# Kernel tuning notes

Hardware: AMD Instinct MI355X
Metric: run time of the kernel (lower is better)

Reference implementation:

```python
import jax, jax.numpy as jnp
import numpy as np

MEMORY_SIZE = 2000
SHAPE = (512, 8, 8)
D = int(np.prod(SHAPE))  # 32768
LAM = 0.0005  # hard-shrink threshold (1/memory_size convention)
EPS = 1e-12   # F.normalize eps


def _l2_normalize(x, axis):
    # matches F.normalize(p=2): x / max(||x||, eps)
    n = jnp.sqrt(jnp.sum(x * x, axis=axis, keepdims=True))
    return x / jnp.maximum(n, EPS)


def _hard_shrink(x):
    return jnp.where(jnp.abs(x) > LAM, x, jnp.zeros_like(x))


def setup_inputs() -> dict:
    key = jax.random.key(0)
    k1, k2 = jax.random.split(key)
    feature = jax.random.normal(k1, (256, *SHAPE), dtype=jnp.float32)
    memory = jax.random.normal(k2, (MEMORY_SIZE, D), dtype=jnp.float32)
    return {"feature": feature, "memory": memory}


def reference(feature, memory):
    B = feature.shape[0]
    flat = feature.reshape(B, -1)                     # [B, D]
    fn = _l2_normalize(flat, axis=1)                  # [B, D]
    mn = _l2_normalize(memory, axis=1)                # [M, D]
    w = jnp.einsum('bd,md->bm', fn, mn)               # cosine similarity [B, M]
    w = jax.nn.softmax(w, axis=1)
    w = _hard_shrink(w)
    w = jax.nn.softmax(w, axis=1)
    mem_feat = jnp.einsum('bm,md->bd', w, memory)     # [B, D]
    mem_feat = mem_feat.reshape(B, *SHAPE)
    return (mem_feat, w)
```

## Files before the change

kernel.cpp:

```cpp
#include <hip/hip_runtime.h>
#include <math.h>


#define D_DIM 32768
#define B_DIM 256
#define M_DIM 2000
#define M_PAD 2048
#define NSPLIT 16
#define LAM 0.0005f
#define LDA 72

typedef __attribute__((ext_vector_type(8))) short bf16x8;
typedef __attribute__((ext_vector_type(4))) float f32x4;

__device__ __forceinline__ unsigned short f2bf(float f) {
  union { float f; unsigned u; } v; v.f = f;
  unsigned r = v.u + 0x7FFFu + ((v.u >> 16) & 1u);
  return (unsigned short)(r >> 16);
}

__global__ __launch_bounds__(256) void prep_kernel(const float* __restrict__ src,
                                                   unsigned short* __restrict__ dst,
                                                   float* __restrict__ rn_inv) {
  const size_t row = blockIdx.x;
  const int t = threadIdx.x;
  const float4* p = (const float4*)(src + row * (size_t)D_DIM);
  ushort4* q = (ushort4*)(dst + row * (size_t)D_DIM);
  float s = 0.f;
  for (int i = t; i < D_DIM / 4; i += 256) {
    float4 v = p[i];
    s = fmaf(v.x, v.x, s); s = fmaf(v.y, v.y, s);
    s = fmaf(v.z, v.z, s); s = fmaf(v.w, v.w, s);
    ushort4 b; b.x = f2bf(v.x); b.y = f2bf(v.y); b.z = f2bf(v.z); b.w = f2bf(v.w);
    q[i] = b;
  }
  #pragma unroll
  for (int off = 32; off > 0; off >>= 1) s += __shfl_down(s, off, 64);
  __shared__ float partial[4];
  if ((t & 63) == 0) partial[t >> 6] = s;
  __syncthreads();
  if (t == 0) {
    float tt = partial[0] + partial[1] + partial[2] + partial[3];
    rn_inv[row] = 1.0f / fmaxf(sqrtf(tt), 1e-12f);
  }
}

__global__ __launch_bounds__(256) void gemm1_kernel(const unsigned short* __restrict__ A,
                                                    const unsigned short* __restrict__ Bm,
                                                    float* __restrict__ Spart) {
  __shared__ __align__(16) unsigned short Asm[256 * LDA];
  __shared__ __align__(16) unsigned short Bsm[64 * LDA];
  const int t = threadIdx.x;
  const int n0 = blockIdx.x * 64;
  const int kbase = blockIdx.y * (D_DIM / NSPLIT);
  const int wid = t >> 6, lane = t & 63;
  const int lr = lane & 15, kq = lane >> 4;
  const int sr = t >> 3;
  const int sc = (t & 7) * 8;

  f32x4 acc[4][4] = {};

  for (int kk = 0; kk < D_DIM / NSPLIT; kk += 64) {
    const size_t kg = (size_t)(kbase + kk + sc);
    __syncthreads();
    #pragma unroll
    for (int i = 0; i < 8; i++) {
      const int r = sr + 32 * i;
      const bf16x8 v = *(const bf16x8*)(A + (size_t)r * D_DIM + kg);
      *(bf16x8*)&Asm[r * LDA + sc] = v;
    }
    #pragma unroll
    for (int i = 0; i < 2; i++) {
      const int r = sr + 32 * i;
      const bf16x8 v = *(const bf16x8*)(Bm + (size_t)(n0 + r) * D_DIM + kg);
      *(bf16x8*)&Bsm[r * LDA + sc] = v;
    }
    __syncthreads();
    bf16x8 bfr[4][2];
    #pragma unroll
    for (int ni = 0; ni < 4; ni++)
      #pragma unroll
      for (int h = 0; h < 2; h++)
        bfr[ni][h] = *(const bf16x8*)&Bsm[(ni * 16 + lr) * LDA + h * 32 + kq * 8];
    #pragma unroll
    for (int mi = 0; mi < 4; mi++) {
      #pragma unroll
      for (int h = 0; h < 2; h++) {
        const bf16x8 af = *(const bf16x8*)&Asm[(wid * 64 + mi * 16 + lr) * LDA + h * 32 + kq * 8];
        #pragma unroll
        for (int ni = 0; ni < 4; ni++)
          acc[mi][ni] = __builtin_amdgcn_mfma_f32_16x16x32_bf16(af, bfr[ni][h], acc[mi][ni], 0, 0, 0);
      }
    }
  }
  float* Sp = Spart + (size_t)blockIdx.y * (B_DIM * M_PAD);
  #pragma unroll
  for (int mi = 0; mi < 4; mi++) {
    const int row0 = wid * 64 + mi * 16 + kq * 4;
    #pragma unroll
    for (int ni = 0; ni < 4; ni++) {
      const int col = n0 + ni * 16 + lr;
      #pragma unroll
      for (int j = 0; j < 4; j++)
        Sp[(size_t)(row0 + j) * M_PAD + col] = acc[mi][ni][j];
    }
  }
}

__device__ __forceinline__ float block_reduce(float x, bool is_max, float* red,
                                              int wid, int lane) {
  #pragma unroll
  for (int off = 32; off > 0; off >>= 1) {
    float o = __shfl_down(x, off, 64);
    x = is_max ? fmaxf(x, o) : (x + o);
  }
  __syncthreads();
  if (lane == 0) red[wid] = x;
  __syncthreads();
  return is_max ? fmaxf(fmaxf(red[0], red[1]), fmaxf(red[2], red[3]))
                : (red[0] + red[1] + red[2] + red[3]);
}

__global__ __launch_bounds__(256) void softmax_kernel(const float* __restrict__ Spart,
                                                      const float* __restrict__ rnf,
                                                      const float* __restrict__ rnm,
                                                      float* __restrict__ wout,
                                                      unsigned short* __restrict__ wbf) {
  const int b = blockIdx.x;
  const int t = threadIdx.x;
  const int wid = t >> 6, lane = t & 63;
  const float sf = rnf[b];
  __shared__ float red[4];

  float v[8];
  #pragma unroll
  for (int i = 0; i < 8; i++) {
    const int m = t + 256 * i;
    float a = 0.f;
    #pragma unroll
    for (int s = 0; s < NSPLIT; s++)
      a += Spart[(size_t)s * (B_DIM * M_PAD) + (size_t)b * M_PAD + m];
    v[i] = (m < M_DIM) ? a * (sf * rnm[m]) : -INFINITY;
  }
  float mx = v[0];
  #pragma unroll
  for (int i = 1; i < 8; i++) mx = fmaxf(mx, v[i]);
  mx = block_reduce(mx, true, red, wid, lane);

  float e[8]; float sum = 0.f;
  #pragma unroll
  for (int i = 0; i < 8; i++) { e[i] = expf(v[i] - mx); sum += e[i]; }
  sum = block_reduce(sum, false, red, wid, lane);
  const float inv = 1.f / sum;

  float s2[8];
  #pragma unroll
  for (int i = 0; i < 8; i++) {
    float w1 = e[i] * inv;
    s2[i] = (w1 > LAM) ? w1 : 0.f;
  }
  float mx2 = 0.f;
  #pragma unroll
  for (int i = 0; i < 8; i++) mx2 = fmaxf(mx2, s2[i]);
  mx2 = block_reduce(mx2, true, red, wid, lane);

  float e2[8]; float sum2 = 0.f;
  #pragma unroll
  for (int i = 0; i < 8; i++) {
    const int m = t + 256 * i;
    e2[i] = (m < M_DIM) ? expf(s2[i] - mx2) : 0.f;
    sum2 += e2[i];
  }
  sum2 = block_reduce(sum2, false, red, wid, lane);
  const float inv2 = 1.f / sum2;

  #pragma unroll
  for (int i = 0; i < 8; i++) {
    const int m = t + 256 * i;
    const float w2 = e2[i] * inv2;
    if (m < M_DIM) wout[(size_t)b * M_DIM + m] = w2;
    wbf[(size_t)b * M_PAD + m] = f2bf(w2);
  }
}

__global__ __launch_bounds__(256) void gemm2_kernel(const unsigned short* __restrict__ W,
                                                    const unsigned short* __restrict__ Bm,
                                                    float* __restrict__ C) {
  __shared__ __align__(16) unsigned short Wsm[256 * LDA];
  __shared__ __align__(16) unsigned short Bt[64 * LDA];
  const int t = threadIdx.x;
  const int n0 = blockIdx.x * 64;
  const int wid = t >> 6, lane = t & 63;
  const int lr = lane & 15, kq = lane >> 4;
  const int sr = t >> 3, sc = (t & 7) * 8;
  const int bk = t >> 4;
  const int bnc = (t & 15) * 4;

  f32x4 acc[4][4] = {};

  for (int k0 = 0; k0 < M_PAD; k0 += 64) {
    __syncthreads();
    #pragma unroll
    for (int i = 0; i < 8; i++) {
      const int r = sr + 32 * i;
      const bf16x8 v = *(const bf16x8*)(W + (size_t)r * M_PAD + k0 + sc);
      *(bf16x8*)&Wsm[r * LDA + sc] = v;
    }
    #pragma unroll
    for (int i = 0; i < 4; i++) {
      const int kl = bk + 16 * i;
      const ushort4 v = *(const ushort4*)(Bm + (size_t)(k0 + kl) * D_DIM + n0 + bnc);
      Bt[(bnc + 0) * LDA + kl] = v.x;
      Bt[(bnc + 1) * LDA + kl] = v.y;
      Bt[(bnc + 2) * LDA + kl] = v.z;
      Bt[(bnc + 3) * LDA + kl] = v.w;
    }
    __syncthreads();
    bf16x8 bfr[4][2];
    #pragma unroll
    for (int ni = 0; ni < 4; ni++)
      #pragma unroll
      for (int h = 0; h < 2; h++)
        bfr[ni][h] = *(const bf16x8*)&Bt[(ni * 16 + lr) * LDA + h * 32 + kq * 8];
    #pragma unroll
    for (int mi = 0; mi < 4; mi++) {
      #pragma unroll
      for (int h = 0; h < 2; h++) {
        const bf16x8 af = *(const bf16x8*)&Wsm[(wid * 64 + mi * 16 + lr) * LDA + h * 32 + kq * 8];
        #pragma unroll
        for (int ni = 0; ni < 4; ni++)
          acc[mi][ni] = __builtin_amdgcn_mfma_f32_16x16x32_bf16(af, bfr[ni][h], acc[mi][ni], 0, 0, 0);
      }
    }
  }
  #pragma unroll
  for (int mi = 0; mi < 4; mi++) {
    const int row0 = wid * 64 + mi * 16 + kq * 4;
    #pragma unroll
    for (int ni = 0; ni < 4; ni++) {
      const int col = n0 + ni * 16 + lr;
      #pragma unroll
      for (int j = 0; j < 4; j++)
        C[(size_t)(row0 + j) * D_DIM + col] = acc[mi][ni][j];
    }
  }
}

extern "C" void kernel_launch(void* const* d_in, const int* in_sizes, int n_in,
                              void* d_out, int out_size, void* d_ws, size_t ws_size,
                              hipStream_t stream) {
  const float* feature = (const float*)d_in[0];
  const float* memory  = (const float*)d_in[1];
  float* out_feat = (float*)d_out;
  float* out_w = out_feat + (size_t)B_DIM * D_DIM;

  char* ws = (char*)d_ws;
  unsigned short* Mem16 = (unsigned short*)ws;
  unsigned short* F16   = (unsigned short*)(ws + 134217728);
  float* Spart          = (float*)(ws + 150994944);
  unsigned short* Wbf   = (unsigned short*)(ws + 184549376);
  float* rnm            = (float*)(ws + 185597952);
  float* rnf            = (float*)(ws + 185606144);

  prep_kernel<<<M_DIM, 256, 0, stream>>>(memory, Mem16, rnm);
  prep_kernel<<<B_DIM, 256, 0, stream>>>(feature, F16, rnf);
  gemm1_kernel<<<dim3(32, NSPLIT), 256, 0, stream>>>(F16, Mem16, Spart);
  softmax_kernel<<<B_DIM, 256, 0, stream>>>(Spart, rnf, rnm, out_w, Wbf);
  gemm2_kernel<<<D_DIM / 64, 256, 0, stream>>>(Wbf, Mem16, out_feat);
}
```

Before: 563.0 us.

## Pre-transpose memory for GEMM2 and use swizzled async global-to-LDS loads

Memory preprocessing is now a tiled kernel that writes both the row-major bf16 copy and a transposed (D x M_PAD) bf16 copy. Row norms are accumulated with atomics into a squared-norm buffer that a new zero kernel clears first. Both GEMMs share a core that loads tiles with global_load_lds 16-byte async copies into XOR-swizzled unpadded LDS. This removes GEMM2's scalar LDS transpose, and the split-K count for GEMM1 is doubled. The trade-off is an extra 128MB transposed write in prep, a larger partial-sum buffer for softmax to reduce, and the reliance on the gfx950 LDS-load intrinsic.

```diff
diff --git a/kernel.cpp b/kernel.cpp
--- a/kernel.cpp
+++ b/kernel.cpp
@@ -6,12 +6,19 @@
 #define B_DIM 256
 #define M_DIM 2000
 #define M_PAD 2048
-#define NSPLIT 16
+#define NSPLIT 32
 #define LAM 0.0005f
-#define LDA 72
 
 typedef __attribute__((ext_vector_type(8))) short bf16x8;
 typedef __attribute__((ext_vector_type(4))) float f32x4;
+
+#define GLOBAL_AS __attribute__((address_space(1)))
+#define LDS_AS __attribute__((address_space(3)))
+
+__device__ __forceinline__ void cp_async16(const void* g, void* l) {
+  __builtin_amdgcn_global_load_lds((const GLOBAL_AS unsigned int*)g,
+                                   (LDS_AS unsigned int*)l, 16, 0, 0);
+}
 
 __device__ __forceinline__ unsigned short f2bf(float f) {
   union { float f; unsigned u; } v; v.f = f;
@@ -19,9 +26,14 @@
   return (unsigned short)(r >> 16);
 }
 
-__global__ __launch_bounds__(256) void prep_kernel(const float* __restrict__ src,
-                                                   unsigned short* __restrict__ dst,
-                                                   float* __restrict__ rn_inv) {
+__global__ __launch_bounds__(256) void zero_kernel(float* __restrict__ p, int n) {
+  int i = blockIdx.x * 256 + threadIdx.x;
+  if (i < n) p[i] = 0.f;
+}
+
+__global__ __launch_bounds__(256) void prep_feat_kernel(const float* __restrict__ src,
+                                                        unsigned short* __restrict__ dst,
+                                                        float* __restrict__ rn_inv) {
   const size_t row = blockIdx.x;
   const int t = threadIdx.x;
   const float4* p = (const float4*)(src + row * (size_t)D_DIM);
@@ -45,54 +57,120 @@
   }
 }
 
+#define LT_S 70
+__global__ __launch_bounds__(256) void prep_mem_kernel(const float* __restrict__ src,
+                                                       unsigned short* __restrict__ Mem16,
+                                                       unsigned short* __restrict__ MemT,
+                                                       float* __restrict__ rnm_sq) {
+  __shared__ __align__(16) unsigned short LT[64 * LT_S];
+  const int t = threadIdx.x;
+  const int m0 = blockIdx.y * 64;
+  const int d0 = blockIdx.x * 256;
+  const int rrow = t >> 4;
+  const int c4 = (t & 15) * 4;
+  float nacc[4] = {0.f, 0.f, 0.f, 0.f};
+
+  for (int sub = 0; sub < 4; sub++) {
+    const int d = d0 + sub * 64;
+    __syncthreads();
+    #pragma unroll
+    for (int p = 0; p < 4; p++) {
+      const int mr = rrow + 16 * p;
+      const int m = m0 + mr;
+      float4 v = make_float4(0.f, 0.f, 0.f, 0.f);
+      if (m < M_DIM) v = *(const float4*)(src + (size_t)m * D_DIM + d + c4);
+      nacc[p] = fmaf(v.x, v.x, fmaf(v.y, v.y, fmaf(v.z, v.z, fmaf(v.w, v.w, nacc[p]))));
+      ushort4 b; b.x = f2bf(v.x); b.y = f2bf(v.y); b.z = f2bf(v.z); b.w = f2bf(v.w);
+      *(ushort4*)&Mem16[(size_t)m * D_DIM + d + c4] = b;
+      *(ushort4*)&LT[mr * LT_S + c4] = b;
+    }
+    __syncthreads();
+    #pragma unroll
+    for (int p = 0; p < 4; p++) {
+      const int dl = rrow + 16 * p;
+      ushort4 o;
+      o.x = LT[(c4 + 0) * LT_S + dl];
+      o.y = LT[(c4 + 1) * LT_S + dl];
+      o.z = LT[(c4 + 2) * LT_S + dl];
+      o.w = LT[(c4 + 3) * LT_S + dl];
+      *(ushort4*)&MemT[(size_t)(d + dl) * M_PAD + m0 + c4] = o;
+    }
+  }
+  #pragma unroll
+  for (int p = 0; p < 4; p++) {
+    float s = nacc[p];
+    #pragma unroll
+    for (int off = 8; off > 0; off >>= 1) s += __shfl_down(s, off, 16);
+    if ((t & 15) == 0) {
+      const int m = m0 + rrow + 16 * p;
+      if (m < M_DIM) atomicAdd(&rnm_sq[m], s);
+    }
+  }
+}
+
+template <int KTILES>
+__device__ __forceinline__ void gemm_core(const unsigned short* __restrict__ A,
+                                          const unsigned short* __restrict__ B,
+                                          size_t lda, size_t ldb,
+                                          unsigned short* Asm, unsigned short* Bsm,
+                                          f32x4 acc[4][4]) {
+  const int t = threadIdx.x;
+  const int wid = t >> 6, lane = t & 63;
+  const int lr = lane & 15, kq = lane >> 4;
+  const int l8 = lane & 7, lrow = lane >> 3;
+  const int sw_stage = (l8 ^ lrow) * 8;
+
+  const unsigned short* Ab = A + (size_t)(64 * wid + lrow) * lda + sw_stage;
+  const unsigned short* Bb = B + (size_t)(16 * wid + lrow) * ldb + sw_stage;
+
+  for (int kt = 0; kt < KTILES; kt++) {
+    const int kk = kt * 64;
+    __syncthreads();
+    #pragma unroll
+    for (int i = 0; i < 8; i++)
+      cp_async16(Ab + kk + (size_t)(8 * i) * lda, &Asm[(64 * wid + 8 * i) * 64]);
+    #pragma unroll
+    for (int i = 0; i < 2; i++)
+      cp_async16(Bb + kk + (size_t)(8 * i) * ldb, &Bsm[(16 * wid + 8 * i) * 64]);
+    __syncthreads();
+
+    bf16x8 bfr[2][4];
+    #pragma unroll
+    for (int h = 0; h < 2; h++) {
+      const int sw = ((h * 4 + kq) ^ (lr & 7)) * 8;
+      #pragma unroll
+      for (int ni = 0; ni < 4; ni++)
+        bfr[h][ni] = *(const bf16x8*)&Bsm[(ni * 16 + lr) * 64 + sw];
+    }
+    #pragma unroll
+    for (int mi = 0; mi < 4; mi++) {
+      #pragma unroll
+      for (int h = 0; h < 2; h++) {
+        const int sw = ((h * 4 + kq) ^ (lr & 7)) * 8;
+        const bf16x8 af = *(const bf16x8*)&Asm[(wid * 64 + mi * 16 + lr) * 64 + sw];
+        #pragma unroll
+        for (int ni = 0; ni < 4; ni++)
+          acc[mi][ni] = __builtin_amdgcn_mfma_f32_16x16x32_bf16(af, bfr[h][ni], acc[mi][ni], 0, 0, 0);
+      }
+    }
+  }
+}
+
 __global__ __launch_bounds__(256) void gemm1_kernel(const unsigned short* __restrict__ A,
                                                     const unsigned short* __restrict__ Bm,
                                                     float* __restrict__ Spart) {
-  __shared__ __align__(16) unsigned short Asm[256 * LDA];
-  __shared__ __align__(16) unsigned short Bsm[64 * LDA];
+  __shared__ __align__(16) unsigned short Asm[256 * 64];
+  __shared__ __align__(16) unsigned short Bsm[64 * 64];
   const int t = threadIdx.x;
   const int n0 = blockIdx.x * 64;
   const int kbase = blockIdx.y * (D_DIM / NSPLIT);
   const int wid = t >> 6, lane = t & 63;
   const int lr = lane & 15, kq = lane >> 4;
-  const int sr = t >> 3;
-  const int sc = (t & 7) * 8;
 
   f32x4 acc[4][4] = {};
-
-  for (int kk = 0; kk < D_DIM / NSPLIT; kk += 64) {
-    const size_t kg = (size_t)(kbase + kk + sc);
-    __syncthreads();
-    #pragma unroll
-    for (int i = 0; i < 8; i++) {
-      const int r = sr + 32 * i;
-      const bf16x8 v = *(const bf16x8*)(A + (size_t)r * D_DIM + kg);
-      *(bf16x8*)&Asm[r * LDA + sc] = v;
-    }
-    #pragma unroll
-    for (int i = 0; i < 2; i++) {
-      const int r = sr + 32 * i;
-      const bf16x8 v = *(const bf16x8*)(Bm + (size_t)(n0 + r) * D_DIM + kg);
-      *(bf16x8*)&Bsm[r * LDA + sc] = v;
-    }
-    __syncthreads();
-    bf16x8 bfr[4][2];
-    #pragma unroll
-    for (int ni = 0; ni < 4; ni++)
-      #pragma unroll
-      for (int h = 0; h < 2; h++)
-        bfr[ni][h] = *(const bf16x8*)&Bsm[(ni * 16 + lr) * LDA + h * 32 + kq * 8];
-    #pragma unroll
-    for (int mi = 0; mi < 4; mi++) {
-      #pragma unroll
-      for (int h = 0; h < 2; h++) {
-        const bf16x8 af = *(const bf16x8*)&Asm[(wid * 64 + mi * 16 + lr) * LDA + h * 32 + kq * 8];
-        #pragma unroll
-        for (int ni = 0; ni < 4; ni++)
-          acc[mi][ni] = __builtin_amdgcn_mfma_f32_16x16x32_bf16(af, bfr[ni][h], acc[mi][ni], 0, 0, 0);
-      }
-    }
-  }
+  gemm_core<(D_DIM / NSPLIT) / 64>(A + kbase, Bm + (size_t)n0 * D_DIM + kbase,
+                                   D_DIM, D_DIM, Asm, Bsm, acc);
+
   float* Sp = Spart + (size_t)blockIdx.y * (B_DIM * M_PAD);
   #pragma unroll
   for (int mi = 0; mi < 4; mi++) {
@@ -107,6 +185,32 @@
   }
 }
 
+__global__ __launch_bounds__(256) void gemm2_kernel(const unsigned short* __restrict__ W,
+                                                    const unsigned short* __restrict__ Bt,
+                                                    float* __restrict__ C) {
+  __shared__ __align__(16) unsigned short Asm[256 * 64];
+  __shared__ __align__(16) unsigned short Bsm[64 * 64];
+  const int t = threadIdx.x;
+  const int n0 = blockIdx.x * 64;
+  const int wid = t >> 6, lane = t & 63;
+  const int lr = lane & 15, kq = lane >> 4;
+
+  f32x4 acc[4][4] = {};
+  gemm_core<M_PAD / 64>(W, Bt + (size_t)n0 * M_PAD, M_PAD, M_PAD, Asm, Bsm, acc);
+
+  #pragma unroll
+  for (int mi = 0; mi < 4; mi++) {
+    const int row0 = wid * 64 + mi * 16 + kq * 4;
+    #pragma unroll
+    for (int ni = 0; ni < 4; ni++) {
+      const int col = n0 + ni * 16 + lr;
+      #pragma unroll
+      for (int j = 0; j < 4; j++)
+        C[(size_t)(row0 + j) * D_DIM + col] = acc[mi][ni][j];
+    }
+  }
+}
+
 __device__ __forceinline__ float block_reduce(float x, bool is_max, float* red,
                                               int wid, int lane) {
   #pragma unroll
@@ -123,7 +227,7 @@
 
 __global__ __launch_bounds__(256) void softmax_kernel(const float* __restrict__ Spart,
                                                       const float* __restrict__ rnf,
-                                                      const float* __restrict__ rnm,
+                                                      const float* __restrict__ rnm_sq,
                                                       float* __restrict__ wout,
                                                       unsigned short* __restrict__ wbf) {
   const int b = blockIdx.x;
@@ -140,7 +244,8 @@
     #pragma unroll
     for (int s = 0; s < NSPLIT; s++)
       a += Spart[(size_t)s * (B_DIM * M_PAD) + (size_t)b * M_PAD + m];
-    v[i] = (m < M_DIM) ? a * (sf * rnm[m]) : -INFINITY;
+    const float mscale = 1.0f / fmaxf(sqrtf(rnm_sq[m]), 1e-12f);
+    v[i] = (m < M_DIM) ? a * (sf * mscale) : -INFINITY;
   }
   float mx = v[0];
   #pragma unroll
@@ -180,69 +285,6 @@
     const float w2 = e2[i] * inv2;
     if (m < M_DIM) wout[(size_t)b * M_DIM + m] = w2;
     wbf[(size_t)b * M_PAD + m] = f2bf(w2);
-  }
-}
-
-__global__ __launch_bounds__(256) void gemm2_kernel(const unsigned short* __restrict__ W,
-                                                    const unsigned short* __restrict__ Bm,
-                                                    float* __restrict__ C) {
-  __shared__ __align__(16) unsigned short Wsm[256 * LDA];
-  __shared__ __align__(16) unsigned short Bt[64 * LDA];
-  const int t = threadIdx.x;
-  const int n0 = blockIdx.x * 64;
-  const int wid = t >> 6, lane = t & 63;
-  const int lr = lane & 15, kq = lane >> 4;
-  const int sr = t >> 3, sc = (t & 7) * 8;
-  const int bk = t >> 4;
-  const int bnc = (t & 15) * 4;
-
-  f32x4 acc[4][4] = {};
-
-  for (int k0 = 0; k0 < M_PAD; k0 += 64) {
-    __syncthreads();
-    #pragma unroll
-    for (int i = 0; i < 8; i++) {
-      const int r = sr + 32 * i;
-      const bf16x8 v = *(const bf16x8*)(W + (size_t)r * M_PAD + k0 + sc);
-      *(bf16x8*)&Wsm[r * LDA + sc] = v;
-    }
-    #pragma unroll
-    for (int i = 0; i < 4; i++) {
-      const int kl = bk + 16 * i;
-      const ushort4 v = *(const ushort4*)(Bm + (size_t)(k0 + kl) * D_DIM + n0 + bnc);
-      Bt[(bnc + 0) * LDA + kl] = v.x;
-      Bt[(bnc + 1) * LDA + kl] = v.y;
-      Bt[(bnc + 2) * LDA + kl] = v.z;
-      Bt[(bnc + 3) * LDA + kl] = v.w;
-    }
-    __syncthreads();
-    bf16x8 bfr[4][2];
-    #pragma unroll
-    for (int ni = 0; ni < 4; ni++)
-      #pragma unroll
-      for (int h = 0; h < 2; h++)
-        bfr[ni][h] = *(const bf16x8*)&Bt[(ni * 16 + lr) * LDA + h * 32 + kq * 8];
-    #pragma unroll
-    for (int mi = 0; mi < 4; mi++) {
-      #pragma unroll
-      for (int h = 0; h < 2; h++) {
-        const bf16x8 af = *(const bf16x8*)&Wsm[(wid * 64 + mi * 16 + lr) * LDA + h * 32 + kq * 8];
-        #pragma unroll
-        for (int ni = 0; ni < 4; ni++)
-          acc[mi][ni] = __builtin_amdgcn_mfma_f32_16x16x32_bf16(af, bfr[ni][h], acc[mi][ni], 0, 0, 0);
-      }
-    }
-  }
-  #pragma unroll
-  for (int mi = 0; mi < 4; mi++) {
-    const int row0 = wid * 64 + mi * 16 + kq * 4;
-    #pragma unroll
-    for (int ni = 0; ni < 4; ni++) {
-      const int col = n0 + ni * 16 + lr;
-      #pragma unroll
-      for (int j = 0; j < 4; j++)
-        C[(size_t)(row0 + j) * D_DIM + col] = acc[mi][ni][j];
-    }
   }
 }
 
@@ -256,15 +298,17 @@
 
   char* ws = (char*)d_ws;
   unsigned short* Mem16 = (unsigned short*)ws;
-  unsigned short* F16   = (unsigned short*)(ws + 134217728);
-  float* Spart          = (float*)(ws + 150994944);
-  unsigned short* Wbf   = (unsigned short*)(ws + 184549376);
-  float* rnm            = (float*)(ws + 185597952);
-  float* rnf            = (float*)(ws + 185606144);
-
-  prep_kernel<<<M_DIM, 256, 0, stream>>>(memory, Mem16, rnm);
-  prep_kernel<<<B_DIM, 256, 0, stream>>>(feature, F16, rnf);
-  gemm1_kernel<<<dim3(32, NSPLIT), 256, 0, stream>>>(F16, Mem16, Spart);
-  softmax_kernel<<<B_DIM, 256, 0, stream>>>(Spart, rnf, rnm, out_w, Wbf);
-  gemm2_kernel<<<D_DIM / 64, 256, 0, stream>>>(Wbf, Mem16, out_feat);
-}
+  unsigned short* MemT  = (unsigned short*)(ws + 134217728ull);
+  unsigned short* F16   = (unsigned short*)(ws + 268435456ull);
+  unsigned short* Wbf   = (unsigned short*)(ws + 285212672ull);
+  float* Spart          = (float*)(ws + 286261248ull);
+  float* rnm_sq         = (float*)(ws + 353370112ull);
+  float* rnf            = (float*)(ws + 353378304ull);
+
+  zero_kernel<<<(M_PAD + 255) / 256, 256, 0, stream>>>(rnm_sq, M_PAD);
+  prep_feat_kernel<<<B_DIM, 256, 0, stream>>>(feature, F16, rnf);
+  prep_mem_kernel<<<dim3(D_DIM / 256, 32), 256, 0, stream>>>(memory, Mem16, MemT, rnm_sq);
+  gemm1_kernel<<<dim3(M_PAD / 64, NSPLIT), 256, 0, stream>>>(F16, Mem16, Spart);
+  softmax_kernel<<<B_DIM, 256, 0, stream>>>(Spart, rnf, rnm_sq, out_w, Wbf);
+  gemm2_kernel<<<D_DIM / 64, 256, 0, stream>>>(Wbf, MemT, out_feat);
+}
```

New measurement: 613.1 us. 1.09x slower.

## Fuse memory bf16 conversion and norm into GEMM1, add async LDS loads

Applied to the files above, without the earlier changes.

The separate prep pass over the fp32 memory matrix is removed. GEMM1 now reads fp32 memory directly, converts it to bf16 in registers, writes the bf16 copy for GEMM2, and accumulates squared row norms with atomics that the softmax kernel turns into inverse norms. The activation and weight tiles in both GEMMs are loaded with global_load_lds into an XOR-swizzled unpadded LDS layout. GEMM2's transpose stores now pack pairs of k values into 32-bit LDS writes. The aim is to avoid re-reading the bf16 memory copy and to cut load-instruction and LDS-store overhead, at the cost of heavier fp32 traffic inside GEMM1, atomic norm accumulation, and an extra zeroing launch.

```diff
diff --git a/kernel.cpp b/kernel.cpp
--- a/kernel.cpp
+++ b/kernel.cpp
@@ -6,12 +6,21 @@
 #define B_DIM 256
 #define M_DIM 2000
 #define M_PAD 2048
-#define NSPLIT 16
+#define NS1 16
+#define KSLAB (D_DIM / NS1)
 #define LAM 0.0005f
-#define LDA 72
+#define LDB 72
 
 typedef __attribute__((ext_vector_type(8))) short bf16x8;
 typedef __attribute__((ext_vector_type(4))) float f32x4;
+
+#define GLOBAL_AS __attribute__((address_space(1)))
+#define LDS_AS __attribute__((address_space(3)))
+
+__device__ __forceinline__ void cp_async16(const void* g, void* l) {
+  __builtin_amdgcn_global_load_lds((const GLOBAL_AS unsigned int*)g,
+                                   (LDS_AS unsigned int*)l, 16, 0, 0);
+}
 
 __device__ __forceinline__ unsigned short f2bf(float f) {
   union { float f; unsigned u; } v; v.f = f;
@@ -19,9 +28,14 @@
   return (unsigned short)(r >> 16);
 }
 
-__global__ __launch_bounds__(256) void prep_kernel(const float* __restrict__ src,
-                                                   unsigned short* __restrict__ dst,
-                                                   float* __restrict__ rn_inv) {
+__global__ __launch_bounds__(256) void zero_kernel(float* __restrict__ p, int n) {
+  int i = blockIdx.x * 256 + threadIdx.x;
+  if (i < n) p[i] = 0.f;
+}
+
+__global__ __launch_bounds__(256) void prep_feat_kernel(const float* __restrict__ src,
+                                                        unsigned short* __restrict__ dst,
+                                                        float* __restrict__ rn_inv) {
   const size_t row = blockIdx.x;
   const int t = threadIdx.x;
   const float4* p = (const float4*)(src + row * (size_t)D_DIM);
@@ -45,64 +59,94 @@
   }
 }
 
-__global__ __launch_bounds__(256) void gemm1_kernel(const unsigned short* __restrict__ A,
-                                                    const unsigned short* __restrict__ Bm,
-                                                    float* __restrict__ Spart) {
-  __shared__ __align__(16) unsigned short Asm[256 * LDA];
-  __shared__ __align__(16) unsigned short Bsm[64 * LDA];
+__global__ __launch_bounds__(256) void gemm1_fused(const unsigned short* __restrict__ F16,
+                                                   const float* __restrict__ mem,
+                                                   unsigned short* __restrict__ Mem16,
+                                                   float* __restrict__ Spart,
+                                                   float* __restrict__ rnm_sq) {
+  __shared__ __align__(16) unsigned short Asm[256 * 64];
+  __shared__ __align__(16) unsigned short Bsm[64 * LDB];
   const int t = threadIdx.x;
-  const int n0 = blockIdx.x * 64;
-  const int kbase = blockIdx.y * (D_DIM / NSPLIT);
+  const int m0 = blockIdx.x * 64;
+  const int kbase = blockIdx.y * KSLAB;
   const int wid = t >> 6, lane = t & 63;
   const int lr = lane & 15, kq = lane >> 4;
-  const int sr = t >> 3;
-  const int sc = (t & 7) * 8;
+  const int l8 = lane & 7, lrow = lane >> 3;
+
+  const int brow = t >> 2;
+  const int bcol = (t & 3) * 16;
+  const int gm = m0 + brow;
+  const bool bvalid = gm < M_DIM;
+  const float* Bg = mem + (size_t)gm * D_DIM + kbase + bcol;
+  unsigned short* M16g = Mem16 + (size_t)gm * D_DIM + kbase + bcol;
+
+  const unsigned short* Ab = F16 + (size_t)(64 * wid + lrow) * D_DIM + kbase + (l8 ^ lrow) * 8;
 
   f32x4 acc[4][4] = {};
-
-  for (int kk = 0; kk < D_DIM / NSPLIT; kk += 64) {
-    const size_t kg = (size_t)(kbase + kk + sc);
+  float ss = 0.f;
+
+  for (int kt = 0; kt < KSLAB / 64; kt++) {
+    const int kk = kt * 64;
     __syncthreads();
     #pragma unroll
-    for (int i = 0; i < 8; i++) {
-      const int r = sr + 32 * i;
-      const bf16x8 v = *(const bf16x8*)(A + (size_t)r * D_DIM + kg);
-      *(bf16x8*)&Asm[r * LDA + sc] = v;
-    }
-    #pragma unroll
-    for (int i = 0; i < 2; i++) {
-      const int r = sr + 32 * i;
-      const bf16x8 v = *(const bf16x8*)(Bm + (size_t)(n0 + r) * D_DIM + kg);
-      *(bf16x8*)&Bsm[r * LDA + sc] = v;
-    }
+    for (int i = 0; i < 8; i++)
+      cp_async16(Ab + kk + (size_t)(8 * i) * D_DIM, &Asm[(64 * wid + 8 * i) * 64]);
+
+    float4 v[4];
+    #pragma unroll
+    for (int j = 0; j < 4; j++)
+      v[j] = bvalid ? *(const float4*)(Bg + kk + 4 * j) : make_float4(0.f, 0.f, 0.f, 0.f);
+    ushort4 c[4];
+    #pragma unroll
+    for (int j = 0; j < 4; j++) {
+      ss = fmaf(v[j].x, v[j].x, ss); ss = fmaf(v[j].y, v[j].y, ss);
+      ss = fmaf(v[j].z, v[j].z, ss); ss = fmaf(v[j].w, v[j].w, ss);
+      c[j].x = f2bf(v[j].x); c[j].y = f2bf(v[j].y);
+      c[j].z = f2bf(v[j].z); c[j].w = f2bf(v[j].w);
+    }
+    *(ushort4*)&Bsm[brow * LDB + bcol + 0]  = c[0];
+    *(ushort4*)&Bsm[brow * LDB + bcol + 4]  = c[1];
+    *(ushort4*)&Bsm[brow * LDB + bcol + 8]  = c[2];
+    *(ushort4*)&Bsm[brow * LDB + bcol + 12] = c[3];
+    *(ushort4*)(M16g + kk + 0)  = c[0];
+    *(ushort4*)(M16g + kk + 4)  = c[1];
+    *(ushort4*)(M16g + kk + 8)  = c[2];
+    *(ushort4*)(M16g + kk + 12) = c[3];
     __syncthreads();
-    bf16x8 bfr[4][2];
-    #pragma unroll
-    for (int ni = 0; ni < 4; ni++)
-      #pragma unroll
-      for (int h = 0; h < 2; h++)
-        bfr[ni][h] = *(const bf16x8*)&Bsm[(ni * 16 + lr) * LDA + h * 32 + kq * 8];
+
+    bf16x8 bfr[2][4];
+    #pragma unroll
+    for (int h = 0; h < 2; h++)
+      #pragma unroll
+      for (int ni = 0; ni < 4; ni++)
+        bfr[h][ni] = *(const bf16x8*)&Bsm[(ni * 16 + lr) * LDB + h * 32 + kq * 8];
     #pragma unroll
     for (int mi = 0; mi < 4; mi++) {
       #pragma unroll
       for (int h = 0; h < 2; h++) {
-        const bf16x8 af = *(const bf16x8*)&Asm[(wid * 64 + mi * 16 + lr) * LDA + h * 32 + kq * 8];
+        const int sw = ((h * 4 + kq) ^ (lr & 7)) * 8;
+        const bf16x8 af = *(const bf16x8*)&Asm[(wid * 64 + mi * 16 + lr) * 64 + sw];
         #pragma unroll
         for (int ni = 0; ni < 4; ni++)
-          acc[mi][ni] = __builtin_amdgcn_mfma_f32_16x16x32_bf16(af, bfr[ni][h], acc[mi][ni], 0, 0, 0);
+          acc[mi][ni] = __builtin_amdgcn_mfma_f32_16x16x32_bf16(af, bfr[h][ni], acc[mi][ni], 0, 0, 0);
       }
     }
   }
+
+  ss += __shfl_down(ss, 2, 4);
+  ss += __shfl_down(ss, 1, 4);
+  if ((t & 3) == 0 && bvalid) atomicAdd(&rnm_sq[gm], ss);
+
   float* Sp = Spart + (size_t)blockIdx.y * (B_DIM * M_PAD);
   #pragma unroll
   for (int mi = 0; mi < 4; mi++) {
-    const int row0 = wid * 64 + mi * 16 + kq * 4;
+    const int b0 = wid * 64 + mi * 16 + kq * 4;
     #pragma unroll
     for (int ni = 0; ni < 4; ni++) {
-      const int col = n0 + ni * 16 + lr;
+      const int col = m0 + ni * 16 + lr;
       #pragma unroll
       for (int j = 0; j < 4; j++)
-        Sp[(size_t)(row0 + j) * M_PAD + col] = acc[mi][ni][j];
+        Sp[(size_t)(b0 + j) * M_PAD + col] = acc[mi][ni][j];
     }
   }
 }
@@ -123,7 +167,7 @@
 
 __global__ __launch_bounds__(256) void softmax_kernel(const float* __restrict__ Spart,
                                                       const float* __restrict__ rnf,
-                                                      const float* __restrict__ rnm,
+                                                      const float* __restrict__ rnm_sq,
                                                       float* __restrict__ wout,
                                                       unsigned short* __restrict__ wbf) {
   const int b = blockIdx.x;
@@ -138,9 +182,10 @@
     const int m = t + 256 * i;
     float a = 0.f;
     #pragma unroll
-    for (int s = 0; s < NSPLIT; s++)
+    for (int s = 0; s < NS1; s++)
       a += Spart[(size_t)s * (B_DIM * M_PAD) + (size_t)b * M_PAD + m];
-    v[i] = (m < M_DIM) ? a * (sf * rnm[m]) : -INFINITY;
+    const float mscale = 1.0f / fmaxf(sqrtf(rnm_sq[m]), 1e-12f);
+    v[i] = (m < M_DIM) ? a * (sf * mscale) : -INFINITY;
   }
   float mx = v[0];
   #pragma unroll
@@ -186,62 +231,69 @@
 __global__ __launch_bounds__(256) void gemm2_kernel(const unsigned short* __restrict__ W,
                                                     const unsigned short* __restrict__ Bm,
                                                     float* __restrict__ C) {
-  __shared__ __align__(16) unsigned short Wsm[256 * LDA];
-  __shared__ __align__(16) unsigned short Bt[64 * LDA];
+  __shared__ __align__(16) unsigned short Wsm[256 * 64];
+  __shared__ __align__(16) unsigned short Bt[64 * LDB];
   const int t = threadIdx.x;
   const int n0 = blockIdx.x * 64;
   const int wid = t >> 6, lane = t & 63;
   const int lr = lane & 15, kq = lane >> 4;
-  const int sr = t >> 3, sc = (t & 7) * 8;
-  const int bk = t >> 4;
-  const int bnc = (t & 15) * 4;
+  const int l8 = lane & 7, lrow = lane >> 3;
+
+  const unsigned short* Wb = W + (size_t)(64 * wid + lrow) * M_PAD + (l8 ^ lrow) * 8;
+
+  const int kl2 = 2 * (t >> 4);
+  const int d4 = (t & 15) * 4;
 
   f32x4 acc[4][4] = {};
 
   for (int k0 = 0; k0 < M_PAD; k0 += 64) {
     __syncthreads();
     #pragma unroll
-    for (int i = 0; i < 8; i++) {
-      const int r = sr + 32 * i;
-      const bf16x8 v = *(const bf16x8*)(W + (size_t)r * M_PAD + k0 + sc);
-      *(bf16x8*)&Wsm[r * LDA + sc] = v;
-    }
-    #pragma unroll
-    for (int i = 0; i < 4; i++) {
-      const int kl = bk + 16 * i;
-      const ushort4 v = *(const ushort4*)(Bm + (size_t)(k0 + kl) * D_DIM + n0 + bnc);
-      Bt[(bnc + 0) * LDA + kl] = v.x;
-      Bt[(bnc + 1) * LDA + kl] = v.y;
-      Bt[(bnc + 2) * LDA + kl] = v.z;
-      Bt[(bnc + 3) * LDA + kl] = v.w;
+    for (int i = 0; i < 8; i++)
+      cp_async16(Wb + k0 + (size_t)(8 * i) * M_PAD, &Wsm[(64 * wid + 8 * i) * 64]);
+    #pragma unroll
+    for (int it = 0; it < 2; it++) {
+      const int kl = kl2 + 32 * it;
+      const ushort4 va = *(const ushort4*)(Bm + (size_t)(k0 + kl) * D_DIM + n0 + d4);
+      const ushort4 vb = *(const ushort4*)(Bm + (size_t)(k0 + kl + 1) * D_DIM + n0 + d4);
+      const unsigned p0 = (unsigned)va.x | ((unsigned)vb.x << 16);
+      const unsigned p1 = (unsigned)va.y | ((unsigned)vb.y << 16);
+      const unsigned p2 = (unsigned)va.z | ((unsigned)vb.z << 16);
+      const unsigned p3 = (unsigned)va.w | ((unsigned)vb.w << 16);
+      *(unsigned*)&Bt[(d4 + 0) * LDB + kl] = p0;
+      *(unsigned*)&Bt[(d4 + 1) * LDB + kl] = p1;
+      *(unsigned*)&Bt[(d4 + 2) * LDB + kl] = p2;
+      *(unsigned*)&Bt[(d4 + 3) * LDB + kl] = p3;
     }
     __syncthreads();
-    bf16x8 bfr[4][2];
-    #pragma unroll
-    for (int ni = 0; ni < 4; ni++)
-      #pragma unroll
-      for (int h = 0; h < 2; h++)
-        bfr[ni][h] = *(const bf16x8*)&Bt[(ni * 16 + lr) * LDA + h * 32 + kq * 8];
+
+    bf16x8 bfr[2][4];
+    #pragma unroll
+    for (int h = 0; h < 2; h++)
+      #pragma unroll
+      for (int ni = 0; ni < 4; ni++)
+        bfr[h][ni] = *(const bf16x8*)&Bt[(ni * 16 + lr) * LDB + h * 32 + kq * 8];
     #pragma unroll
     for (int mi = 0; mi < 4; mi++) {
       #pragma unroll
       for (int h = 0; h < 2; h++) {
-        const bf16x8 af = *(const bf16x8*)&Wsm[(wid * 64 + mi * 16 + lr) * LDA + h * 32 + kq * 8];
+        const int sw = ((h * 4 + kq) ^ (lr & 7)) * 8;
+        const bf16x8 af = *(const bf16x8*)&Wsm[(wid * 64 + mi * 16 + lr) * 64 + sw];
         #pragma unroll
         for (int ni = 0; ni < 4; ni++)
-          acc[mi][ni] = __builtin_amdgcn_mfma_f32_16x16x32_bf16(af, bfr[ni][h], acc[mi][ni], 0, 0, 0);
+          acc[mi][ni] = __builtin_amdgcn_mfma_f32_16x16x32_bf16(af, bfr[h][ni], acc[mi][ni], 0, 0, 0);
       }
     }
   }
   #pragma unroll
   for (int mi = 0; mi < 4; mi++) {
-    const int row0 = wid * 64 + mi * 16 + kq * 4;
+    const int b0 = wid * 64 + mi * 16 + kq * 4;
     #pragma unroll
     for (int ni = 0; ni < 4; ni++) {
       const int col = n0 + ni * 16 + lr;
       #pragma unroll
       for (int j = 0; j < 4; j++)
-        C[(size_t)(row0 + j) * D_DIM + col] = acc[mi][ni][j];
+        C[(size_t)(b0 + j) * D_DIM + col] = acc[mi][ni][j];
     }
   }
 }
@@ -256,15 +308,15 @@
 
   char* ws = (char*)d_ws;
   unsigned short* Mem16 = (unsigned short*)ws;
-  unsigned short* F16   = (unsigned short*)(ws + 134217728);
-  float* Spart          = (float*)(ws + 150994944);
-  unsigned short* Wbf   = (unsigned short*)(ws + 184549376);
-  float* rnm            = (float*)(ws + 185597952);
-  float* rnf            = (float*)(ws + 185606144);
-
-  prep_kernel<<<M_DIM, 256, 0, stream>>>(memory, Mem16, rnm);
-  prep_kernel<<<B_DIM, 256, 0, stream>>>(feature, F16, rnf);
-  gemm1_kernel<<<dim3(32, NSPLIT), 256, 0, stream>>>(F16, Mem16, Spart);
-  softmax_kernel<<<B_DIM, 256, 0, stream>>>(Spart, rnf, rnm, out_w, Wbf);
+  unsigned short* F16   = (unsigned short*)(ws + 134217728ull);
+  unsigned short* Wbf   = (unsigned short*)(ws + 150994944ull);
+  float* Spart          = (float*)(ws + 152043520ull);
+  float* rnm_sq         = (float*)(ws + 185597952ull);
+  float* rnf            = (float*)(ws + 185606144ull);
+
+  zero_kernel<<<(M_PAD + 255) / 256, 256, 0, stream>>>(rnm_sq, M_PAD);
+  prep_feat_kernel<<<B_DIM, 256, 0, stream>>>(feature, F16, rnf);
+  gemm1_fused<<<dim3(M_PAD / 64, NS1), 256, 0, stream>>>(F16, memory, Mem16, Spart, rnm_sq);
+  softmax_kernel<<<B_DIM, 256, 0, stream>>>(Spart, rnf, rnm_sq, out_w, Wbf);
   gemm2_kernel<<<D_DIM / 64, 256, 0, stream>>>(Wbf, Mem16, out_feat);
 }
```

Result: faster. 519.9 us (-7.7%).
